# Kernel tuning notes

Hardware: AMD Instinct MI355X
Metric: run time of the kernel (lower is better)

Reference implementation:

```python
import jax, jax.numpy as jnp
import numpy as np

B, T, I, H, O = 4096, 512, 1, 64, 3

def setup_inputs() -> dict:
    key = jax.random.key(0)
    ks = jax.random.split(key, 7)
    s = 1.0 / np.sqrt(H)  # torch default LSTM init scale
    return {
        "x": jax.random.normal(ks[0], (B, T, I), dtype=jnp.float32),
        "W_ih": jax.random.uniform(ks[1], (4 * H, I), jnp.float32, -s, s),
        "W_hh": jax.random.uniform(ks[2], (4 * H, H), jnp.float32, -s, s),
        "b_ih": jax.random.uniform(ks[3], (4 * H,), jnp.float32, -s, s),
        "b_hh": jax.random.uniform(ks[4], (4 * H,), jnp.float32, -s, s),
        "W_out": jax.random.uniform(ks[5], (O, H), jnp.float32, -s, s),
        "b_out": jax.random.uniform(ks[6], (O,), jnp.float32, -s, s),
    }

def reference(x, W_ih, W_hh, b_ih, b_hh, W_out, b_out):
    # Single-layer LSTM (PyTorch gate order i,f,g,o), zero initial state,
    # then linear head applied to the last hidden state (== r_out[:, -1, :]).
    b = b_ih + b_hh
    Bsz, Hh = x.shape[0], W_hh.shape[1]
    # Precompute input projections for all timesteps: [T, B, 4H]
    x_proj = jnp.einsum('bti,gi->tbg', x, W_ih) + b

    def step(carry, xp_t):
        h, c = carry
        gates = xp_t + h @ W_hh.T  # [B, 4H]
        i, f, g, o = jnp.split(gates, 4, axis=-1)
        c_new = jax.nn.sigmoid(f) * c + jax.nn.sigmoid(i) * jnp.tanh(g)
        h_new = jax.nn.sigmoid(o) * jnp.tanh(c_new)
        return (h_new, c_new), None

    h0 = jnp.zeros((Bsz, Hh), x.dtype)
    (h_last, _), _ = jax.lax.scan(step, (h0, h0), x_proj)
    return h_last @ W_out.T + b_out  # [B, 3]
```

## Files before the change

### kernel.cpp

```cpp
#include <hip/hip_runtime.h>

#define BATCH 4096
#define TT 512
#define HH 64
#define BT 8
#define XS 516
#define HS 72

typedef __attribute__((ext_vector_type(8))) short short8;
typedef __attribute__((ext_vector_type(4))) float floatx4;

__device__ __forceinline__ unsigned short f2bf(float f) {
    unsigned u = __float_as_uint(f);
    u = u + 0x7FFFu + ((u >> 16) & 1u);
    return (unsigned short)(u >> 16);
}

__global__ __launch_bounds__(256, 2) void lstm_kernel(
    const float* __restrict__ x, const float* __restrict__ W_ih,
    const float* __restrict__ W_hh, const float* __restrict__ b_ih,
    const float* __restrict__ b_hh, const float* __restrict__ W_out,
    const float* __restrict__ b_out, float* __restrict__ out)
{
    __shared__ __align__(16) float x_s[BT * XS];
    __shared__ __align__(16) unsigned short hb0[16 * HS];
    __shared__ __align__(16) unsigned short hb1[16 * HS];
    __shared__ __align__(16) float hf[BT * 65];

    const int tid = threadIdx.x;
    const int w = tid >> 6;
    const int l = tid & 63;
    const int q = l >> 4;
    const int c = l & 15;
    const int n = 16 * w + c;
    const int bbase = blockIdx.x * BT;

    for (int i = 0; i < 4; ++i) {
        int flat = i * 256 + tid;
        int row = flat >> 7, c4 = flat & 127;
        const float4* xg = reinterpret_cast<const float4*>(x + (size_t)(bbase + row) * TT);
        float4 v = xg[c4];
        *reinterpret_cast<float4*>(&x_s[row * XS + c4 * 4]) = v;
    }
    for (int i = tid; i < 16 * HS; i += 256) { hb0[i] = 0; hb1[i] = 0; }

    const float L1 = 1.44269504089f;
    const float L2 = 2.88539008178f;

    short8 bfr[4][2];
    float wih[4], bb[4];
    for (int t = 0; t < 4; ++t) {
        float sc = (t == 2) ? L2 : -L1;
        int g = 64 * t + n;
        wih[t] = W_ih[g] * sc;
        bb[t] = (b_ih[g] + b_hh[g]) * sc;
        for (int ks = 0; ks < 2; ++ks) {
            const float* wp = W_hh + g * 64 + ks * 32 + q * 8;
            short8 v;
            #pragma unroll
            for (int j = 0; j < 8; ++j) v[j] = (short)f2bf(wp[j] * sc);
            bfr[t][ks] = v;
        }
    }

    float cst[2] = {0.f, 0.f};
    float hvk[2] = {0.f, 0.f};

    floatx4 acc[4];
    #pragma unroll
    for (int t = 0; t < 4; ++t) acc[t] = floatx4{0.f, 0.f, 0.f, 0.f};

    const int aoff = c * HS + q * 8;
    const int woff = (4 * q) * HS + n;
    const float* xrowA = &x_s[(2 * q) * XS];
    const float* xrowB = &x_s[(2 * q + 1) * XS];

    __syncthreads();

    if (blockIdx.x >= (BATCH / BT / 2)) __builtin_amdgcn_s_sleep(9);

    for (int ts4 = 0; ts4 < TT; ts4 += 4) {
        float4 xa = *reinterpret_cast<const float4*>(xrowA + ts4);
        float4 xb = *reinterpret_cast<const float4*>(xrowB + ts4);
        #pragma unroll
        for (int u = 0; u < 4; ++u) {
            const unsigned short* src = (u & 1) ? hb1 : hb0;
            unsigned short* dst = (u & 1) ? hb0 : hb1;

            short8 a0 = *reinterpret_cast<const short8*>(src + aoff);
            short8 a1 = *reinterpret_cast<const short8*>(src + aoff + 32);

            float x0 = (&xa.x)[u], x1 = (&xb.x)[u];
            #pragma unroll
            for (int t = 0; t < 4; ++t) {
                acc[t][0] = fmaf(x0, wih[t], bb[t]);
                acc[t][1] = fmaf(x1, wih[t], bb[t]);
            }

            #pragma unroll
            for (int t = 0; t < 4; ++t) {
                acc[t] = __builtin_amdgcn_mfma_f32_16x16x32_bf16(a0, bfr[t][0], acc[t], 0, 0, 0);
                acc[t] = __builtin_amdgcn_mfma_f32_16x16x32_bf16(a1, bfr[t][1], acc[t], 0, 0, 0);
            }

            #pragma unroll
            for (int rr = 0; rr < 2; ++rr) {
                float ei = __builtin_amdgcn_exp2f(acc[0][rr]);
                float ef = __builtin_amdgcn_exp2f(acc[1][rr]);
                float eg = __builtin_amdgcn_exp2f(acc[2][rr]);
                float eo = __builtin_amdgcn_exp2f(acc[3][rr]);
                float pf1 = 1.f + ef, pig = (1.f + ei) * (1.f + eg);
                float num = fmaf(cst[rr], pig, (eg - 1.f) * pf1);
                cst[rr] = num * __builtin_amdgcn_rcpf(pf1 * pig);
                float ec = __builtin_amdgcn_exp2f(L2 * cst[rr]);
                float hv = (ec - 1.f) * __builtin_amdgcn_rcpf((1.f + eo) * (1.f + ec));
                hvk[rr] = hv;
                dst[woff + rr * HS] = f2bf(hv);
            }
            __syncthreads();
        }
    }

    hf[(2 * q) * 65 + n] = hvk[0];
    hf[(2 * q + 1) * 65 + n] = hvk[1];
    __syncthreads();

    if (tid < BT * 3) {
        int row = tid / 3, o = tid % 3;
        float s = b_out[o];
        #pragma unroll 8
        for (int k = 0; k < HH; ++k) s = fmaf(hf[row * 65 + k], W_out[o * 64 + k], s);
        out[(size_t)(bbase + row) * 3 + o] = s;
    }
}

extern "C" void kernel_launch(void* const* d_in, const int* in_sizes, int n_in,
                              void* d_out, int out_size, void* d_ws, size_t ws_size,
                              hipStream_t stream) {
    const float* x     = (const float*)d_in[0];
    const float* W_ih  = (const float*)d_in[1];
    const float* W_hh  = (const float*)d_in[2];
    const float* b_ih  = (const float*)d_in[3];
    const float* b_hh  = (const float*)d_in[4];
    const float* W_out = (const float*)d_in[5];
    const float* b_out = (const float*)d_in[6];
    float* out = (float*)d_out;
    hipLaunchKernelGGL(lstm_kernel, dim3(BATCH / BT), dim3(256), 0, stream,
                       x, W_ih, W_hh, b_ih, b_hh, W_out, b_out, out);
}
```

Before: 284.0 us.

## Rotate LSTM step loop, batch reciprocals across rows, drop staggered sleep

Rotates the recurrence so that each iteration computes the gate nonlinearities first, writes h, syncs, then issues the next step's MFMAs. The last step is peeled into an epilogue. The two rows share a single reciprocal through the product trick, which cuts the rcp instructions on the serial critical path from four to two per step. It also removes the s_sleep stagger for the second half of the blocks and the float4 x unroll, so x is now read as a scalar each step. The shared reciprocal risks overflow or underflow when the product of the two denominators is extreme, and the buffer ping-pong changes accordingly.

```diff
diff --git a/kernel.cpp b/kernel.cpp
--- a/kernel.cpp
+++ b/kernel.cpp
@@ -77,48 +77,89 @@
 
     __syncthreads();
 
-    if (blockIdx.x >= (BATCH / BT / 2)) __builtin_amdgcn_s_sleep(9);
+    {
+        float x0 = xrowA[0], x1 = xrowB[0];
+        #pragma unroll
+        for (int t = 0; t < 4; ++t) {
+            acc[t][0] = fmaf(x0, wih[t], bb[t]);
+            acc[t][1] = fmaf(x1, wih[t], bb[t]);
+        }
+    }
 
-    for (int ts4 = 0; ts4 < TT; ts4 += 4) {
-        float4 xa = *reinterpret_cast<const float4*>(xrowA + ts4);
-        float4 xb = *reinterpret_cast<const float4*>(xrowB + ts4);
+    for (int k = 0; k < TT - 1; ++k) {
+        unsigned short* dst = (k & 1) ? hb1 : hb0;
+
+        float ei0 = __builtin_amdgcn_exp2f(acc[0][0]);
+        float ef0 = __builtin_amdgcn_exp2f(acc[1][0]);
+        float eg0 = __builtin_amdgcn_exp2f(acc[2][0]);
+        float eo0 = __builtin_amdgcn_exp2f(acc[3][0]);
+        float ei1 = __builtin_amdgcn_exp2f(acc[0][1]);
+        float ef1 = __builtin_amdgcn_exp2f(acc[1][1]);
+        float eg1 = __builtin_amdgcn_exp2f(acc[2][1]);
+        float eo1 = __builtin_amdgcn_exp2f(acc[3][1]);
+
+        float pf0 = 1.f + ef0, pg0 = (1.f + ei0) * (1.f + eg0);
+        float pf1 = 1.f + ef1, pg1 = (1.f + ei1) * (1.f + eg1);
+        float d0 = pf0 * pg0, d1 = pf1 * pg1;
+        float rd = __builtin_amdgcn_rcpf(d0 * d1);
+        float num0 = fmaf(cst[0], pg0, (eg0 - 1.f) * pf0);
+        float num1 = fmaf(cst[1], pg1, (eg1 - 1.f) * pf1);
+        cst[0] = num0 * d1 * rd;
+        cst[1] = num1 * d0 * rd;
+
+        float ec0 = __builtin_amdgcn_exp2f(L2 * cst[0]);
+        float ec1 = __builtin_amdgcn_exp2f(L2 * cst[1]);
+        float e0 = (1.f + eo0) * (1.f + ec0);
+        float e1 = (1.f + eo1) * (1.f + ec1);
+        float re = __builtin_amdgcn_rcpf(e0 * e1);
+        hvk[0] = (ec0 - 1.f) * e1 * re;
+        hvk[1] = (ec1 - 1.f) * e0 * re;
+
+        dst[woff] = f2bf(hvk[0]);
+        dst[woff + HS] = f2bf(hvk[1]);
+
+        float xa = xrowA[k + 1], xb = xrowB[k + 1];
+
+        __syncthreads();
+
+        short8 a0 = *reinterpret_cast<const short8*>(dst + aoff);
+        short8 a1 = *reinterpret_cast<const short8*>(dst + aoff + 32);
         #pragma unroll
-        for (int u = 0; u < 4; ++u) {
-            const unsigned short* src = (u & 1) ? hb1 : hb0;
-            unsigned short* dst = (u & 1) ? hb0 : hb1;
+        for (int t = 0; t < 4; ++t) {
+            acc[t][0] = fmaf(xa, wih[t], bb[t]);
+            acc[t][1] = fmaf(xb, wih[t], bb[t]);
+        }
+        #pragma unroll
+        for (int t = 0; t < 4; ++t) {
+            acc[t] = __builtin_amdgcn_mfma_f32_16x16x32_bf16(a0, bfr[t][0], acc[t], 0, 0, 0);
+            acc[t] = __builtin_amdgcn_mfma_f32_16x16x32_bf16(a1, bfr[t][1], acc[t], 0, 0, 0);
+        }
+    }
 
-            short8 a0 = *reinterpret_cast<const short8*>(src + aoff);
-            short8 a1 = *reinterpret_cast<const short8*>(src + aoff + 32);
-
-            float x0 = (&xa.x)[u], x1 = (&xb.x)[u];
-            #pragma unroll
-            for (int t = 0; t < 4; ++t) {
-                acc[t][0] = fmaf(x0, wih[t], bb[t]);
-                acc[t][1] = fmaf(x1, wih[t], bb[t]);
-            }
-
-            #pragma unroll
-            for (int t = 0; t < 4; ++t) {
-                acc[t] = __builtin_amdgcn_mfma_f32_16x16x32_bf16(a0, bfr[t][0], acc[t], 0, 0, 0);
-                acc[t] = __builtin_amdgcn_mfma_f32_16x16x32_bf16(a1, bfr[t][1], acc[t], 0, 0, 0);
-            }
-
-            #pragma unroll
-            for (int rr = 0; rr < 2; ++rr) {
-                float ei = __builtin_amdgcn_exp2f(acc[0][rr]);
-                float ef = __builtin_amdgcn_exp2f(acc[1][rr]);
-                float eg = __builtin_amdgcn_exp2f(acc[2][rr]);
-                float eo = __builtin_amdgcn_exp2f(acc[3][rr]);
-                float pf1 = 1.f + ef, pig = (1.f + ei) * (1.f + eg);
-                float num = fmaf(cst[rr], pig, (eg - 1.f) * pf1);
-                cst[rr] = num * __builtin_amdgcn_rcpf(pf1 * pig);
-                float ec = __builtin_amdgcn_exp2f(L2 * cst[rr]);
-                float hv = (ec - 1.f) * __builtin_amdgcn_rcpf((1.f + eo) * (1.f + ec));
-                hvk[rr] = hv;
-                dst[woff + rr * HS] = f2bf(hv);
-            }
-            __syncthreads();
-        }
+    {
+        float ei0 = __builtin_amdgcn_exp2f(acc[0][0]);
+        float ef0 = __builtin_amdgcn_exp2f(acc[1][0]);
+        float eg0 = __builtin_amdgcn_exp2f(acc[2][0]);
+        float eo0 = __builtin_amdgcn_exp2f(acc[3][0]);
+        float ei1 = __builtin_amdgcn_exp2f(acc[0][1]);
+        float ef1 = __builtin_amdgcn_exp2f(acc[1][1]);
+        float eg1 = __builtin_amdgcn_exp2f(acc[2][1]);
+        float eo1 = __builtin_amdgcn_exp2f(acc[3][1]);
+        float pf0 = 1.f + ef0, pg0 = (1.f + ei0) * (1.f + eg0);
+        float pf1 = 1.f + ef1, pg1 = (1.f + ei1) * (1.f + eg1);
+        float d0 = pf0 * pg0, d1 = pf1 * pg1;
+        float rd = __builtin_amdgcn_rcpf(d0 * d1);
+        float num0 = fmaf(cst[0], pg0, (eg0 - 1.f) * pf0);
+        float num1 = fmaf(cst[1], pg1, (eg1 - 1.f) * pf1);
+        cst[0] = num0 * d1 * rd;
+        cst[1] = num1 * d0 * rd;
+        float ec0 = __builtin_amdgcn_exp2f(L2 * cst[0]);
+        float ec1 = __builtin_amdgcn_exp2f(L2 * cst[1]);
+        float e0 = (1.f + eo0) * (1.f + ec0);
+        float e1 = (1.f + eo1) * (1.f + ec1);
+        float re = __builtin_amdgcn_rcpf(e0 * e1);
+        hvk[0] = (ec0 - 1.f) * e1 * re;
+        hvk[1] = (ec1 - 1.f) * e0 * re;
     }
 
     hf[(2 * q) * 65 + n] = hvk[0];
```

New measurement: 270.9 us. 4.6% less time.

## Pack LSTM gate math into float2 ops and restructure step loop

Applied to the files above, without the earlier changes.

The gate activation math for the two rows each thread owns is rewritten as two-wide float vector operations, so the compiler can emit packed FP32 instructions. The two reciprocals per row are merged into one shared reciprocal with a swap trick. The time loop is re-rotated so each step runs activation, writes h, hits one barrier and then issues the MFMAs, with the first step's projection peeled out. It also drops the staggered s_sleep for the second half of the blocks and reads x one scalar per step instead of as float4. The shared reciprocal of a product of large exponentials risks overflow or precision loss.

```diff
diff --git a/kernel.cpp b/kernel.cpp
--- a/kernel.cpp
+++ b/kernel.cpp
@@ -9,6 +9,7 @@
 
 typedef __attribute__((ext_vector_type(8))) short short8;
 typedef __attribute__((ext_vector_type(4))) float floatx4;
+typedef __attribute__((ext_vector_type(2))) float float2v;
 
 __device__ __forceinline__ unsigned short f2bf(float f) {
     unsigned u = __float_as_uint(f);
@@ -48,12 +49,14 @@
     const float L2 = 2.88539008178f;
 
     short8 bfr[4][2];
-    float wih[4], bb[4];
+    float2v wih2[4], bb2[4];
     for (int t = 0; t < 4; ++t) {
         float sc = (t == 2) ? L2 : -L1;
         int g = 64 * t + n;
-        wih[t] = W_ih[g] * sc;
-        bb[t] = (b_ih[g] + b_hh[g]) * sc;
+        float wv = W_ih[g] * sc;
+        float bv = (b_ih[g] + b_hh[g]) * sc;
+        wih2[t] = float2v{wv, wv};
+        bb2[t] = float2v{bv, bv};
         for (int ks = 0; ks < 2; ++ks) {
             const float* wp = W_hh + g * 64 + ks * 32 + q * 8;
             short8 v;
@@ -63,8 +66,10 @@
         }
     }
 
-    float cst[2] = {0.f, 0.f};
-    float hvk[2] = {0.f, 0.f};
+    float2v cst2 = {0.f, 0.f};
+    float2v hv2 = {0.f, 0.f};
+    const float2v one2 = {1.f, 1.f};
+    const float2v L2v = {L2, L2};
 
     floatx4 acc[4];
     #pragma unroll
@@ -77,52 +82,71 @@
 
     __syncthreads();
 
-    if (blockIdx.x >= (BATCH / BT / 2)) __builtin_amdgcn_s_sleep(9);
-
-    for (int ts4 = 0; ts4 < TT; ts4 += 4) {
-        float4 xa = *reinterpret_cast<const float4*>(xrowA + ts4);
-        float4 xb = *reinterpret_cast<const float4*>(xrowB + ts4);
+    {
+        float2v x01 = {xrowA[0], xrowB[0]};
         #pragma unroll
-        for (int u = 0; u < 4; ++u) {
-            const unsigned short* src = (u & 1) ? hb1 : hb0;
-            unsigned short* dst = (u & 1) ? hb0 : hb1;
-
-            short8 a0 = *reinterpret_cast<const short8*>(src + aoff);
-            short8 a1 = *reinterpret_cast<const short8*>(src + aoff + 32);
-
-            float x0 = (&xa.x)[u], x1 = (&xb.x)[u];
-            #pragma unroll
-            for (int t = 0; t < 4; ++t) {
-                acc[t][0] = fmaf(x0, wih[t], bb[t]);
-                acc[t][1] = fmaf(x1, wih[t], bb[t]);
-            }
-
-            #pragma unroll
-            for (int t = 0; t < 4; ++t) {
-                acc[t] = __builtin_amdgcn_mfma_f32_16x16x32_bf16(a0, bfr[t][0], acc[t], 0, 0, 0);
-                acc[t] = __builtin_amdgcn_mfma_f32_16x16x32_bf16(a1, bfr[t][1], acc[t], 0, 0, 0);
-            }
-
-            #pragma unroll
-            for (int rr = 0; rr < 2; ++rr) {
-                float ei = __builtin_amdgcn_exp2f(acc[0][rr]);
-                float ef = __builtin_amdgcn_exp2f(acc[1][rr]);
-                float eg = __builtin_amdgcn_exp2f(acc[2][rr]);
-                float eo = __builtin_amdgcn_exp2f(acc[3][rr]);
-                float pf1 = 1.f + ef, pig = (1.f + ei) * (1.f + eg);
-                float num = fmaf(cst[rr], pig, (eg - 1.f) * pf1);
-                cst[rr] = num * __builtin_amdgcn_rcpf(pf1 * pig);
-                float ec = __builtin_amdgcn_exp2f(L2 * cst[rr]);
-                float hv = (ec - 1.f) * __builtin_amdgcn_rcpf((1.f + eo) * (1.f + ec));
-                hvk[rr] = hv;
-                dst[woff + rr * HS] = f2bf(hv);
-            }
-            __syncthreads();
+        for (int t = 0; t < 4; ++t) {
+            float2v a2 = x01 * wih2[t] + bb2[t];
+            acc[t][0] = a2.x; acc[t][1] = a2.y;
         }
     }
 
-    hf[(2 * q) * 65 + n] = hvk[0];
-    hf[(2 * q + 1) * 65 + n] = hvk[1];
+    #define ACTP() do {                                                         \
+        float2v ei2, ef2, eg2, eo2;                                             \
+        ei2.x = __builtin_amdgcn_exp2f(acc[0][0]);                              \
+        ei2.y = __builtin_amdgcn_exp2f(acc[0][1]);                              \
+        ef2.x = __builtin_amdgcn_exp2f(acc[1][0]);                              \
+        ef2.y = __builtin_amdgcn_exp2f(acc[1][1]);                              \
+        eg2.x = __builtin_amdgcn_exp2f(acc[2][0]);                              \
+        eg2.y = __builtin_amdgcn_exp2f(acc[2][1]);                              \
+        eo2.x = __builtin_amdgcn_exp2f(acc[3][0]);                              \
+        eo2.y = __builtin_amdgcn_exp2f(acc[3][1]);                              \
+        float2v pf2 = ef2 + one2;                                               \
+        float2v pg2 = (ei2 + one2) * (eg2 + one2);                              \
+        float2v d2 = pf2 * pg2;                                                 \
+        float rd = __builtin_amdgcn_rcpf(d2.x * d2.y);                          \
+        float2v num2 = cst2 * pg2 + (eg2 - one2) * pf2;                         \
+        float2v dsw = {d2.y, d2.x};                                             \
+        cst2 = num2 * dsw * rd;                                                 \
+        float2v l2c = cst2 * L2v;                                               \
+        float2v ec2;                                                            \
+        ec2.x = __builtin_amdgcn_exp2f(l2c.x);                                  \
+        ec2.y = __builtin_amdgcn_exp2f(l2c.y);                                  \
+        float2v e2 = (eo2 + one2) * (ec2 + one2);                               \
+        float re = __builtin_amdgcn_rcpf(e2.x * e2.y);                          \
+        float2v esw = {e2.y, e2.x};                                             \
+        hv2 = (ec2 - one2) * esw * re;                                          \
+    } while (0)
+
+    for (int k = 0; k < TT - 1; ++k) {
+        unsigned short* dst = (k & 1) ? hb1 : hb0;
+
+        ACTP();
+        dst[woff] = f2bf(hv2.x);
+        dst[woff + HS] = f2bf(hv2.y);
+
+        float2v x01 = {xrowA[k + 1], xrowB[k + 1]};
+
+        __syncthreads();
+
+        short8 a0 = *reinterpret_cast<const short8*>(dst + aoff);
+        short8 a1 = *reinterpret_cast<const short8*>(dst + aoff + 32);
+        #pragma unroll
+        for (int t = 0; t < 4; ++t) {
+            float2v a2 = x01 * wih2[t] + bb2[t];
+            acc[t][0] = a2.x; acc[t][1] = a2.y;
+        }
+        #pragma unroll
+        for (int t = 0; t < 4; ++t) {
+            acc[t] = __builtin_amdgcn_mfma_f32_16x16x32_bf16(a0, bfr[t][0], acc[t], 0, 0, 0);
+            acc[t] = __builtin_amdgcn_mfma_f32_16x16x32_bf16(a1, bfr[t][1], acc[t], 0, 0, 0);
+        }
+    }
+
+    ACTP();
+
+    hf[(2 * q) * 65 + n] = hv2.x;
+    hf[(2 * q + 1) * 65 + n] = hv2.y;
     __syncthreads();
 
     if (tid < BT * 3) {
@@ -132,6 +156,7 @@
         for (int k = 0; k < HH; ++k) s = fmaf(hf[row * 65 + k], W_out[o * 64 + k], s);
         out[(size_t)(bbase + row) * 3 + o] = s;
     }
+    #undef ACTP
 }
 
 extern "C" void kernel_launch(void* const* d_in, const int* in_sizes, int n_in,
```

New measurement: 257.6 us. 9.3% less time.
